# Kernel optimization log

Hardware: AMD Instinct MI355X
Metric: run time of the kernel (lower is better)

## Reference

```python
import jax, jax.numpy as jnp
import numpy as np

B, S, H = 2, 2048, 2048
E, I, SH = 8, 768, 5632
TOP_K = 2


def setup_inputs() -> dict:
    key = jax.random.key(0)
    ks = jax.random.split(key, 8)
    sc = lambda *shape: 1.0 / np.sqrt(shape[-2] if len(shape) > 1 else 1.0)
    return {
        "hidden_states": jax.random.normal(ks[0], (B, S, H), jnp.float32),
        "router_w": jax.random.normal(ks[1], (H, E), jnp.float32) * (1.0 / np.sqrt(H)),
        "expert_gate_up_w": jax.random.normal(ks[2], (E, H, 2 * I), jnp.float32) * (1.0 / np.sqrt(H)),
        "expert_down_w": jax.random.normal(ks[3], (E, I, H), jnp.float32) * (1.0 / np.sqrt(I)),
        "shared_gate_w": jax.random.normal(ks[4], (H, SH), jnp.float32) * (1.0 / np.sqrt(H)),
        "shared_up_w": jax.random.normal(ks[5], (H, SH), jnp.float32) * (1.0 / np.sqrt(H)),
        "shared_down_w": jax.random.normal(ks[6], (SH, H), jnp.float32) * (1.0 / np.sqrt(SH)),
        "shared_expert_gate_w": jax.random.normal(ks[7], (H, 1), jnp.float32) * (1.0 / np.sqrt(H)),
    }


def reference(hidden_states, router_w, expert_gate_up_w, expert_down_w,
              shared_gate_w, shared_up_w, shared_down_w, shared_expert_gate_w):
    b, s, h = hidden_states.shape
    x = hidden_states.reshape(-1, h)  # [T, H]

    # Shared expert (SwiGLU) gated by sigmoid scalar gate per token.
    gate = jax.nn.silu((x @ shared_gate_w).astype(jnp.float32)).astype(x.dtype)
    shared_out = (gate * (x @ shared_up_w)) @ shared_down_w  # [T, H]
    shared_out = jax.nn.sigmoid(x @ shared_expert_gate_w) * shared_out

    # Router: softmax -> top-k -> renormalize -> dense routing weights [E, T].
    router_logits = x @ router_w  # [T, E]
    router_probs = jax.nn.softmax(router_logits, axis=-1)
    top_p, top_i = jax.lax.top_k(router_probs, TOP_K)  # [T, k]
    top_p = top_p / jnp.sum(top_p, axis=-1, keepdims=True)
    one_hot = jax.nn.one_hot(top_i, E, dtype=top_p.dtype)  # [T, k, E]
    routing_full = jnp.sum(one_hot * top_p[..., None], axis=1)  # [T, E]
    routing_full = routing_full.T.astype(x.dtype)  # [E, T]

    # Dense per-expert SwiGLU over all tokens (as in source einsums).
    gate_up = jnp.einsum('th,ehm->etm', x, expert_gate_up_w)  # [E, T, 2I]
    g, u = jnp.split(gate_up, 2, axis=-1)
    g = jax.nn.silu(g.astype(jnp.float32)).astype(x.dtype)
    expert_out = jnp.einsum('eti,eih->eth', u * g, expert_down_w)  # [E, T, H]

    expert_contribution = jnp.sum(expert_out * routing_full[:, :, None], axis=0)  # [T, H]
    out = (expert_contribution + shared_out).reshape(b, s, h)
    return out, router_logits
```

## Files before the change

### kernel.cpp

```cpp
#include <hip/hip_runtime.h>
#include <hip/hip_bf16.h>
#include <stdint.h>

#define DEVFN static __device__ __forceinline__

typedef __attribute__((ext_vector_type(8))) short bf16x8;
typedef __attribute__((ext_vector_type(4))) float f32x4;
typedef unsigned short u16;
typedef unsigned int u32;
typedef unsigned long long u64;

DEVFN u16 f2bf(float f) {
    union { float f; u32 u; } v; v.f = f;
    u32 r = v.u + 0x7FFFu + ((v.u >> 16) & 1u);
    return (u16)(r >> 16);
}

DEVFN void g2l16(const void* g, void* l) {
    __builtin_amdgcn_global_load_lds(
        (const __attribute__((address_space(1))) u32*)g,
        (__attribute__((address_space(3))) u32*)l, 16, 0, 0);
}

template<int NSLOT>
DEVFN void stage(const u16* __restrict__ src, int ldk, u16* lds, int tid) {
#pragma unroll
    for (int i = 0; i < NSLOT / 256; ++i) {
        int slot = i * 256 + tid;
        int row = slot >> 2, chunk = slot & 3;
        int kg = chunk ^ ((row >> 1) & 3);
        g2l16(src + (long)row * ldk + kg * 8, lds + slot * 8);
    }
}

DEVFN bf16x8 ld_frag(const u16* lds, int row, int kg) {
    int chunk = kg ^ ((row >> 1) & 3);
    const u16* p = lds + row * 32 + chunk * 8;
    return *(const __attribute__((address_space(3))) bf16x8*)p;
}

__global__ __launch_bounds__(256) void gemm_down_k(
    const u16* __restrict__ A, const u16* __restrict__ B,
    float* __restrict__ C, const float* __restrict__ gvec,
    int K, int ldc)
{
    __shared__ u16 sm[2][8192];
    const int tid = threadIdx.x;
    const int lane = tid & 63, wv = tid >> 6;
    const int wm = wv >> 1, wn = wv & 1;
    const int m0 = blockIdx.y * 128, n0 = blockIdx.x * 128;
    const u16* Ab = A + (long)m0 * K;
    const u16* Bb = B + (long)n0 * K;

    f32x4 acc[4][4];
#pragma unroll
    for (int i = 0; i < 4; ++i)
#pragma unroll
        for (int j = 0; j < 4; ++j) acc[i][j] = f32x4{0.f, 0.f, 0.f, 0.f};

    stage<512>(Ab, K, &sm[0][0], tid);
    stage<512>(Bb, K, &sm[0][4096], tid);

    const int nk = K >> 5;
    for (int kt = 0; kt < nk; ++kt) {
        const int cur = kt & 1;
        __syncthreads();
        if (kt + 1 < nk) {
            stage<512>(Ab + (kt + 1) * 32, K, &sm[cur ^ 1][0], tid);
            stage<512>(Bb + (kt + 1) * 32, K, &sm[cur ^ 1][4096], tid);
        }
        const int l15 = lane & 15, kg = lane >> 4;
        bf16x8 av[4], bv[4];
#pragma unroll
        for (int f = 0; f < 4; ++f) {
            av[f] = ld_frag(&sm[cur][0],    wm * 64 + f * 16 + l15, kg);
            bv[f] = ld_frag(&sm[cur][4096], wn * 64 + f * 16 + l15, kg);
        }
#pragma unroll
        for (int fm = 0; fm < 4; ++fm)
#pragma unroll
            for (int fn = 0; fn < 4; ++fn)
                acc[fm][fn] = __builtin_amdgcn_mfma_f32_16x16x32_bf16(
                    av[fm], bv[fn], acc[fm][fn], 0, 0, 0);
    }

    const int l15 = lane & 15, lq = lane >> 4;
#pragma unroll
    for (int fm = 0; fm < 4; ++fm) {
#pragma unroll
        for (int j = 0; j < 4; ++j) {
            int row = m0 + wm * 64 + fm * 16 + lq * 4 + j;
            float gmul = gvec[row];
#pragma unroll
            for (int fn = 0; fn < 4; ++fn) {
                int col = n0 + wn * 64 + fn * 16 + l15;
                C[(long)row * ldc + col] = acc[fm][fn][j] * gmul;
            }
        }
    }
}

__global__ __launch_bounds__(256) void gemm_swiglu_k(
    const u16* __restrict__ A, const u16* __restrict__ Bg,
    const u16* __restrict__ Bu, u16* __restrict__ out, int K, int ldc)
{
    __shared__ u16 sm[2][8192];
    const int tid = threadIdx.x;
    const int lane = tid & 63, wv = tid >> 6;
    const int wm = wv >> 1, wn = wv & 1;
    const int m0 = blockIdx.y * 128, n0 = blockIdx.x * 64;
    const u16* Ab  = A  + (long)m0 * K;
    const u16* Bgb = Bg + (long)n0 * K;
    const u16* Bub = Bu + (long)n0 * K;

    f32x4 ag[4][2], au[4][2];
#pragma unroll
    for (int i = 0; i < 4; ++i)
#pragma unroll
        for (int j = 0; j < 2; ++j) {
            ag[i][j] = f32x4{0.f, 0.f, 0.f, 0.f};
            au[i][j] = f32x4{0.f, 0.f, 0.f, 0.f};
        }

    stage<512>(Ab,  K, &sm[0][0],    tid);
    stage<256>(Bgb, K, &sm[0][4096], tid);
    stage<256>(Bub, K, &sm[0][6144], tid);

    const int nk = K >> 5;
    for (int kt = 0; kt < nk; ++kt) {
        const int cur = kt & 1;
        __syncthreads();
        if (kt + 1 < nk) {
            stage<512>(Ab  + (kt + 1) * 32, K, &sm[cur ^ 1][0],    tid);
            stage<256>(Bgb + (kt + 1) * 32, K, &sm[cur ^ 1][4096], tid);
            stage<256>(Bub + (kt + 1) * 32, K, &sm[cur ^ 1][6144], tid);
        }
        const int l15 = lane & 15, kg = lane >> 4;
        bf16x8 av[4], gv[2], uv[2];
#pragma unroll
        for (int f = 0; f < 4; ++f)
            av[f] = ld_frag(&sm[cur][0], wm * 64 + f * 16 + l15, kg);
#pragma unroll
        for (int f = 0; f < 2; ++f) {
            gv[f] = ld_frag(&sm[cur][4096], wn * 32 + f * 16 + l15, kg);
            uv[f] = ld_frag(&sm[cur][6144], wn * 32 + f * 16 + l15, kg);
        }
#pragma unroll
        for (int fm = 0; fm < 4; ++fm)
#pragma unroll
            for (int fn = 0; fn < 2; ++fn) {
                ag[fm][fn] = __builtin_amdgcn_mfma_f32_16x16x32_bf16(
                    av[fm], gv[fn], ag[fm][fn], 0, 0, 0);
                au[fm][fn] = __builtin_amdgcn_mfma_f32_16x16x32_bf16(
                    av[fm], uv[fn], au[fm][fn], 0, 0, 0);
            }
    }

    const int l15 = lane & 15, lq = lane >> 4;
#pragma unroll
    for (int fm = 0; fm < 4; ++fm) {
#pragma unroll
        for (int j = 0; j < 4; ++j) {
            int row = m0 + wm * 64 + fm * 16 + lq * 4 + j;
#pragma unroll
            for (int fn = 0; fn < 2; ++fn) {
                int col = n0 + wn * 32 + fn * 16 + l15;
                float g = ag[fm][fn][j], u = au[fm][fn][j];
                float s = g * (1.f / (1.f + __expf(-g))) * u;
                out[(long)row * ldc + col] = f2bf(s);
            }
        }
    }
}

__global__ __launch_bounds__(256) void gemm_swiglu_moe_k(
    const u16* __restrict__ xb, const u16* __restrict__ Beg,
    const u16* __restrict__ Beu, const int* __restrict__ tok,
    const int* __restrict__ cntp, u16* __restrict__ eact,
    int K, int I_, int cap)
{
    const int e = blockIdx.z;
    const int m0 = blockIdx.y * 128;
    if (m0 >= cntp[e]) return;
    const int n0 = blockIdx.x * 64;

    __shared__ u16 sm[2][8192];
    const int tid = threadIdx.x;
    const int lane = tid & 63, wv = tid >> 6;
    const int wm = wv >> 1, wn = wv & 1;

    const int rA0 = tid >> 2, rA1 = 64 + (tid >> 2);
    const int* tseg = tok + (long)e * cap + m0;
    const long t0 = tseg[rA0], t1 = tseg[rA1];
    const int kg0 = (tid & 3) ^ ((rA0 >> 1) & 3);
    const int kg1 = (tid & 3) ^ ((rA1 >> 1) & 3);
    const u16* pa0 = xb + t0 * K + kg0 * 8;
    const u16* pa1 = xb + t1 * K + kg1 * 8;

    const u16* Bgb = Beg + ((long)e * I_ + n0) * K;
    const u16* Bub = Beu + ((long)e * I_ + n0) * K;

    f32x4 ag[4][2], au[4][2];
#pragma unroll
    for (int i = 0; i < 4; ++i)
#pragma unroll
        for (int j = 0; j < 2; ++j) {
            ag[i][j] = f32x4{0.f, 0.f, 0.f, 0.f};
            au[i][j] = f32x4{0.f, 0.f, 0.f, 0.f};
        }

    g2l16(pa0, &sm[0][(long)tid * 8]);
    g2l16(pa1, &sm[0][(long)(256 + tid) * 8]);
    stage<256>(Bgb, K, &sm[0][4096], tid);
    stage<256>(Bub, K, &sm[0][6144], tid);

    const int nk = K >> 5;
    for (int kt = 0; kt < nk; ++kt) {
        const int cur = kt & 1;
        __syncthreads();
        if (kt + 1 < nk) {
            g2l16(pa0 + (kt + 1) * 32, &sm[cur ^ 1][(long)tid * 8]);
            g2l16(pa1 + (kt + 1) * 32, &sm[cur ^ 1][(long)(256 + tid) * 8]);
            stage<256>(Bgb + (kt + 1) * 32, K, &sm[cur ^ 1][4096], tid);
            stage<256>(Bub + (kt + 1) * 32, K, &sm[cur ^ 1][6144], tid);
        }
        const int l15 = lane & 15, kg = lane >> 4;
        bf16x8 av[4], gv[2], uv[2];
#pragma unroll
        for (int f = 0; f < 4; ++f)
            av[f] = ld_frag(&sm[cur][0], wm * 64 + f * 16 + l15, kg);
#pragma unroll
        for (int f = 0; f < 2; ++f) {
            gv[f] = ld_frag(&sm[cur][4096], wn * 32 + f * 16 + l15, kg);
            uv[f] = ld_frag(&sm[cur][6144], wn * 32 + f * 16 + l15, kg);
        }
#pragma unroll
        for (int fm = 0; fm < 4; ++fm)
#pragma unroll
            for (int fn = 0; fn < 2; ++fn) {
                ag[fm][fn] = __builtin_amdgcn_mfma_f32_16x16x32_bf16(
                    av[fm], gv[fn], ag[fm][fn], 0, 0, 0);
                au[fm][fn] = __builtin_amdgcn_mfma_f32_16x16x32_bf16(
                    av[fm], uv[fn], au[fm][fn], 0, 0, 0);
            }
    }

    const int l15 = lane & 15, lq = lane >> 4;
#pragma unroll
    for (int fm = 0; fm < 4; ++fm) {
#pragma unroll
        for (int j = 0; j < 4; ++j) {
            long row = (long)e * cap + m0 + wm * 64 + fm * 16 + lq * 4 + j;
#pragma unroll
            for (int fn = 0; fn < 2; ++fn) {
                int col = n0 + wn * 32 + fn * 16 + l15;
                float g = ag[fm][fn][j], u = au[fm][fn][j];
                float s = g * (1.f / (1.f + __expf(-g))) * u;
                eact[row * I_ + col] = f2bf(s);
            }
        }
    }
}

__global__ __launch_bounds__(256) void gemm_down_moe_k(
    const u16* __restrict__ eact, const u16* __restrict__ Bed,
    float* __restrict__ out, const int* __restrict__ tok,
    const float* __restrict__ wrow, const int* __restrict__ cntp,
    int K, int ldc, int cap)
{
    const int e = blockIdx.z;
    const int m0 = blockIdx.y * 128;
    if (m0 >= cntp[e]) return;
    const int n0 = blockIdx.x * 128;

    __shared__ u16 sm[2][8192];
    const int tid = threadIdx.x;
    const int lane = tid & 63, wv = tid >> 6;
    const int wm = wv >> 1, wn = wv & 1;
    const u16* Ab = eact + ((long)e * cap + m0) * K;
    const u16* Bb = Bed + (long)e * ldc * K + (long)n0 * K;

    f32x4 acc[4][4];
#pragma unroll
    for (int i = 0; i < 4; ++i)
#pragma unroll
        for (int j = 0; j < 4; ++j) acc[i][j] = f32x4{0.f, 0.f, 0.f, 0.f};

    stage<512>(Ab, K, &sm[0][0], tid);
    stage<512>(Bb, K, &sm[0][4096], tid);

    const int nk = K >> 5;
    for (int kt = 0; kt < nk; ++kt) {
        const int cur = kt & 1;
        __syncthreads();
        if (kt + 1 < nk) {
            stage<512>(Ab + (kt + 1) * 32, K, &sm[cur ^ 1][0], tid);
            stage<512>(Bb + (kt + 1) * 32, K, &sm[cur ^ 1][4096], tid);
        }
        const int l15 = lane & 15, kg = lane >> 4;
        bf16x8 av[4], bv[4];
#pragma unroll
        for (int f = 0; f < 4; ++f) {
            av[f] = ld_frag(&sm[cur][0],    wm * 64 + f * 16 + l15, kg);
            bv[f] = ld_frag(&sm[cur][4096], wn * 64 + f * 16 + l15, kg);
        }
#pragma unroll
        for (int fm = 0; fm < 4; ++fm)
#pragma unroll
            for (int fn = 0; fn < 4; ++fn)
                acc[fm][fn] = __builtin_amdgcn_mfma_f32_16x16x32_bf16(
                    av[fm], bv[fn], acc[fm][fn], 0, 0, 0);
    }

    const int l15 = lane & 15, lq = lane >> 4;
#pragma unroll
    for (int fm = 0; fm < 4; ++fm) {
#pragma unroll
        for (int j = 0; j < 4; ++j) {
            long crow = (long)e * cap + m0 + wm * 64 + fm * 16 + lq * 4 + j;
            float w = wrow[crow];
            if (w != 0.f) {
                long t = tok[crow];
#pragma unroll
                for (int fn = 0; fn < 4; ++fn) {
                    int col = n0 + wn * 64 + fn * 16 + l15;
                    atomicAdd(out + t * ldc + col, acc[fm][fn][j] * w);
                }
            }
        }
    }
}

__global__ __launch_bounds__(256) void router_k(
    const float* __restrict__ x, const float* __restrict__ rw,
    const float* __restrict__ sgw, float* __restrict__ logits,
    int2* __restrict__ te, float2* __restrict__ tw,
    float* __restrict__ sig, int T, int H)
{
    const int tid = threadIdx.x, lane = tid & 63, wv = tid >> 6;
    const int t = blockIdx.x * 4 + wv;
    const float* xr = x + (long)t * H;
    float acc[8] = {0, 0, 0, 0, 0, 0, 0, 0};
    float as = 0.f;
    for (int h = lane; h < H; h += 64) {
        float xv = xr[h];
        const float* r = rw + h * 8;
#pragma unroll
        for (int e = 0; e < 8; ++e) acc[e] += xv * r[e];
        as += xv * sgw[h];
    }
#pragma unroll
    for (int off = 32; off; off >>= 1) {
#pragma unroll
        for (int e = 0; e < 8; ++e) acc[e] += __shfl_xor(acc[e], off);
        as += __shfl_xor(as, off);
    }
    if (lane == 0) {
        float mx = acc[0];
#pragma unroll
        for (int e = 1; e < 8; ++e) mx = fmaxf(mx, acc[e]);
        float p[8], sum = 0.f;
#pragma unroll
        for (int e = 0; e < 8; ++e) { p[e] = expf(acc[e] - mx); sum += p[e]; }
        int i1 = 0;
#pragma unroll
        for (int e = 1; e < 8; ++e) if (p[e] > p[i1]) i1 = e;
        int i2 = (i1 == 0) ? 1 : 0;
#pragma unroll
        for (int e = 0; e < 8; ++e) if (e != i1 && p[e] > p[i2]) i2 = e;
        float den = p[i1] + p[i2];
        te[t] = make_int2(i1, i2);
        tw[t] = make_float2(p[i1] / den, p[i2] / den);
#pragma unroll
        for (int e = 0; e < 8; ++e) logits[(long)t * 8 + e] = acc[e];
        sig[t] = 1.f / (1.f + expf(-as));
    }
}

__global__ __launch_bounds__(256) void compact_k(
    const int2* __restrict__ te, const float2* __restrict__ tw,
    int* __restrict__ tok, float* __restrict__ wrow,
    int* __restrict__ cntp, int T, int cap)
{
    const int e = blockIdx.x;
    const int tid = threadIdx.x, lane = tid & 63, wv = tid >> 6;
    __shared__ int wtot[4];
    int cnt = 0;
    for (int c0 = 0; c0 < T; c0 += 256) {
        int t = c0 + tid;
        int2 ids = te[t];
        float2 ws = tw[t];
        float w = (ids.x == e) ? ws.x : ((ids.y == e) ? ws.y : -1.f);
        bool sel = (w >= 0.f);
        u64 b = __ballot(sel);
        int rln = __popcll(b & ((1ull << lane) - 1ull));
        if (lane == 0) wtot[wv] = __popcll(b);
        __syncthreads();
        int rank = rln, tot = 0;
#pragma unroll
        for (int k = 0; k < 4; ++k) { if (k < wv) rank += wtot[k]; tot += wtot[k]; }
        if (sel) {
            int pos = cnt + rank;
            if (pos < cap) {
                tok[(long)e * cap + pos] = t;
                wrow[(long)e * cap + pos] = w;
            }
        }
        cnt += tot;
        __syncthreads();
    }
    if (cnt > cap) cnt = cap;
    int cp = (cnt + 127) & ~127;
    for (int p = cnt + tid; p < cp; p += 256) {
        tok[(long)e * cap + p] = 0;
        wrow[(long)e * cap + p] = 0.f;
    }
    if (tid == 0) cntp[e] = cp;
}

__global__ __launch_bounds__(256) void transpose_k(
    const float* __restrict__ src0, long src_zstr, int src_ld,
    u16* __restrict__ dst0, long dst_zstr, int dst_ld)
{
    __shared__ float tile[32][33];
    const float* src = src0 + (long)blockIdx.z * src_zstr;
    u16* dst = dst0 + (long)blockIdx.z * dst_zstr;
    int r0 = blockIdx.y * 32, c0 = blockIdx.x * 32;
    int tx = threadIdx.x, ty = threadIdx.y;
#pragma unroll
    for (int k = 0; k < 4; ++k)
        tile[ty + 8 * k][tx] = src[(long)(r0 + ty + 8 * k) * src_ld + c0 + tx];
    __syncthreads();
#pragma unroll
    for (int k = 0; k < 4; ++k)
        dst[(long)(c0 + ty + 8 * k) * dst_ld + r0 + tx] = f2bf(tile[tx][ty + 8 * k]);
}

__global__ __launch_bounds__(256) void cvt_x_k(const float* __restrict__ x,
                                               u16* __restrict__ xb)
{
    long i = ((long)blockIdx.x * 256 + threadIdx.x) * 4;
    float4 v = *(const float4*)(x + i);
    union { u16 s[4]; uint2 v2; } o;
    o.s[0] = f2bf(v.x); o.s[1] = f2bf(v.y); o.s[2] = f2bf(v.z); o.s[3] = f2bf(v.w);
    *(uint2*)(xb + i) = o.v2;
}

extern "C" void kernel_launch(void* const* d_in, const int* in_sizes, int n_in,
                              void* d_out, int out_size, void* d_ws, size_t ws_size,
                              hipStream_t stream) {
    (void)in_sizes; (void)n_in; (void)out_size; (void)ws_size;
    const int Hd = 2048, E = 8, I = 768, SH = 5632, T = 4096, CAP = 2048;

    const float* x    = (const float*)d_in[0];
    const float* rw   = (const float*)d_in[1];
    const float* egu  = (const float*)d_in[2];
    const float* edw  = (const float*)d_in[3];
    const float* sgw  = (const float*)d_in[4];
    const float* suw  = (const float*)d_in[5];
    const float* sdw  = (const float*)d_in[6];
    const float* segw = (const float*)d_in[7];
    float* out = (float*)d_out;
    float* logits = out + (size_t)T * Hd;

    char* wsp = (char*)d_ws;
    size_t off = 0;
    auto alloc = [&](size_t bytes) {
        void* p = wsp + off; off += (bytes + 255) & ~(size_t)255; return p;
    };
    u16* xb   = (u16*)alloc((size_t)T * Hd * 2);
    u16* Bgs  = (u16*)alloc((size_t)SH * Hd * 2);
    u16* Bus  = (u16*)alloc((size_t)SH * Hd * 2);
    u16* Bds  = (u16*)alloc((size_t)Hd * SH * 2);
    u16* Beg  = (u16*)alloc((size_t)E * I * Hd * 2);
    u16* Beu  = (u16*)alloc((size_t)E * I * Hd * 2);
    u16* Bed  = (u16*)alloc((size_t)E * Hd * I * 2);
    u16* hs   = (u16*)alloc((size_t)T * SH * 2);
    u16* eact = (u16*)alloc((size_t)E * CAP * I * 2);
    int2*   te   = (int2*)alloc((size_t)T * 8);
    float2* tw   = (float2*)alloc((size_t)T * 8);
    int*    tok  = (int*)alloc((size_t)E * CAP * 4);
    float*  wrow = (float*)alloc((size_t)E * CAP * 4);
    int*    cntp = (int*)alloc(64);
    float*  sig  = (float*)alloc((size_t)T * 4);

    dim3 tb(32, 8);
    cvt_x_k<<<(T * Hd) / 1024, 256, 0, stream>>>(x, xb);
    router_k<<<T / 4, 256, 0, stream>>>(x, rw, segw, logits, te, tw, sig, T, Hd);
    compact_k<<<E, 256, 0, stream>>>(te, tw, tok, wrow, cntp, T, CAP);

    transpose_k<<<dim3(SH / 32, Hd / 32), tb, 0, stream>>>(sgw, 0, SH, Bgs, 0, Hd);
    transpose_k<<<dim3(SH / 32, Hd / 32), tb, 0, stream>>>(suw, 0, SH, Bus, 0, Hd);
    transpose_k<<<dim3(Hd / 32, SH / 32), tb, 0, stream>>>(sdw, 0, Hd, Bds, 0, SH);
    transpose_k<<<dim3(I / 32, Hd / 32, E), tb, 0, stream>>>(
        egu, (long)Hd * 2 * I, 2 * I, Beg, (long)I * Hd, Hd);
    transpose_k<<<dim3(I / 32, Hd / 32, E), tb, 0, stream>>>(
        egu + I, (long)Hd * 2 * I, 2 * I, Beu, (long)I * Hd, Hd);
    transpose_k<<<dim3(Hd / 32, I / 32, E), tb, 0, stream>>>(
        edw, (long)I * Hd, Hd, Bed, (long)Hd * I, I);

    gemm_swiglu_k<<<dim3(SH / 64, T / 128), 256, 0, stream>>>(
        xb, Bgs, Bus, hs, Hd, SH);
    gemm_down_k<<<dim3(Hd / 128, T / 128), 256, 0, stream>>>(
        hs, Bds, out, sig, SH, Hd);
    gemm_swiglu_moe_k<<<dim3(I / 64, CAP / 128, E), 256, 0, stream>>>(
        xb, Beg, Beu, tok, cntp, eact, Hd, I, CAP);
    gemm_down_moe_k<<<dim3(Hd / 128, CAP / 128, E), 256, 0, stream>>>(
        eact, Bed, out, tok, wrow, cntp, I, Hd, CAP);
}
```

Before: 656.2 us.

## Replace shared-expert SwiGLU GEMM with 256x128 8-wave pipelined kernel

Replaces the 128x64 double-buffered shared-expert gate/up GEMM with an 8-wave, 256x128 tile kernel using K=64 steps. It uses 128KB of dynamic LDS, an XOR swizzle, and staggered half-tile async loads fenced by explicit vmcnt waits and barriers. It also adds s_setprio around the MFMA blocks and a block-index remap that groups neighbouring tiles. The goal is more data reuse per LDS byte and better overlap of global loads with MFMA. In exchange it relies on hand-tuned waitcnt ordering and drops to low occupancy.

Result: faster. 612.3 us (-6.7%).

```diff
diff --git a/kernel.cpp b/kernel.cpp
--- a/kernel.cpp
+++ b/kernel.cpp
@@ -20,6 +20,153 @@
     __builtin_amdgcn_global_load_lds(
         (const __attribute__((address_space(1))) u32*)g,
         (__attribute__((address_space(3))) u32*)l, 16, 0, 0);
+}
+
+DEVFN void hbar() {
+    __asm__ __volatile__("" ::: "memory");
+    __builtin_amdgcn_s_barrier();
+    __asm__ __volatile__("" ::: "memory");
+}
+DEVFN void vm4() { asm volatile("s_waitcnt vmcnt(4)" ::: "memory"); }
+DEVFN void vm0() { asm volatile("s_waitcnt vmcnt(0)" ::: "memory"); }
+
+__global__ __launch_bounds__(512, 2) void gemm8_swiglu_k(
+    const u16* __restrict__ A, const u16* __restrict__ Bg,
+    const u16* __restrict__ Bu, u16* __restrict__ out,
+    int K, int nx, int ldc)
+{
+    extern __shared__ char smraw[];
+    char* smA = smraw;
+    char* smB = smraw + 65536;
+
+    const int tid = threadIdx.x;
+    const int lane = tid & 63, wv = tid >> 6;
+    const int wm = wv >> 2, wn = wv & 3;
+    const int l15 = lane & 15, kg = lane >> 4;
+
+    const int nwg = gridDim.x;
+    const int id = (blockIdx.x & 7) * (nwg >> 3) + (blockIdx.x >> 3);
+    const int m0 = (id / nx) * 256, n0 = (id % nx) * 128;
+
+    const u16* Ap  = A  + (long)m0 * K;
+    const u16* Bgp = Bg + (long)n0 * K;
+    const u16* Bup = Bu + (long)n0 * K;
+
+    f32x4 accg[8][2], accu[8][2];
+#pragma unroll
+    for (int i = 0; i < 8; ++i)
+#pragma unroll
+        for (int j = 0; j < 2; ++j) {
+            accg[i][j] = f32x4{0.f, 0.f, 0.f, 0.f};
+            accu[i][j] = f32x4{0.f, 0.f, 0.f, 0.f};
+        }
+
+    auto stA = [&](int kt, int hh, int buf) {
+        const u16* src = Ap + ((long)hh * 128) * K + kt * 64;
+        char* dst = smA + buf * 32768 + hh * 16384;
+#pragma unroll
+        for (int i = 0; i < 2; ++i) {
+            int slot = i * 512 + tid;
+            int row = slot >> 3, ch = slot & 7;
+            g2l16(src + (long)row * K + ((ch ^ (row & 7)) << 3), dst + slot * 16);
+        }
+    };
+    auto stB = [&](int kt, int hh, int buf) {
+        const u16* src = (hh ? Bup : Bgp) + kt * 64;
+        char* dst = smB + buf * 32768 + hh * 16384;
+#pragma unroll
+        for (int i = 0; i < 2; ++i) {
+            int slot = i * 512 + tid;
+            int row = slot >> 3, ch = slot & 7;
+            g2l16(src + (long)row * K + ((ch ^ (row & 7)) << 3), dst + slot * 16);
+        }
+    };
+    auto frag = [&](const char* base, int r, int c) -> bf16x8 {
+        return *(const __attribute__((address_space(3))) bf16x8*)
+            (base + r * 128 + ((c ^ (r & 7)) << 4));
+    };
+
+    stA(0, 0, 0); stA(0, 1, 0);
+    stB(0, 0, 0); stB(0, 1, 0);
+    stB(1, 0, 1); stB(1, 1, 1);
+    vm4();
+    hbar();
+
+    const int nk = K >> 6;
+    for (int kt = 0; kt < nk; kt += 2) {
+        const bool more = (kt + 2) < nk;
+#pragma unroll
+        for (int h = 0; h < 2; ++h) {
+            const char* ab = smA + h * 32768;
+            const char* bb = smB + h * 32768;
+            bf16x8 bgv[2][2], buv[2][2];
+#pragma unroll
+            for (int p = 0; p < 4; ++p) {
+                if (p == 0) {
+#pragma unroll
+                    for (int fn = 0; fn < 2; ++fn)
+#pragma unroll
+                        for (int s = 0; s < 2; ++s) {
+                            int rB = wn * 32 + fn * 16 + l15;
+                            bgv[fn][s] = frag(bb, rB, s * 4 + kg);
+                            buv[fn][s] = frag(bb + 16384, rB, s * 4 + kg);
+                        }
+                }
+                bf16x8 av[2][2];
+#pragma unroll
+                for (int am = 0; am < 2; ++am)
+#pragma unroll
+                    for (int s = 0; s < 2; ++s)
+                        av[am][s] = frag(ab, wm * 128 + (p * 2 + am) * 16 + l15,
+                                         s * 4 + kg);
+                if (h == 0) {
+                    if (p == 0)      { stA(kt + 1, 0, 1); stA(kt + 1, 1, 1); }
+                    else if (p == 1) { if (more) stB(kt + 2, 0, 0); }
+                    else if (p == 2) { if (more) stB(kt + 2, 1, 0); }
+                    else             { if (more) vm4(); else vm0(); }
+                } else {
+                    if (more) {
+                        if (p == 0)      stA(kt + 2, 0, 0);
+                        else if (p == 1) stA(kt + 2, 1, 0);
+                        else if (p == 2) stB(kt + 3, 0, 1);
+                        else             { stB(kt + 3, 1, 1); vm4(); }
+                    }
+                }
+                hbar();
+                __builtin_amdgcn_sched_barrier(0);
+                __builtin_amdgcn_s_setprio(1);
+#pragma unroll
+                for (int am = 0; am < 2; ++am)
+#pragma unroll
+                    for (int s = 0; s < 2; ++s)
+#pragma unroll
+                        for (int fn = 0; fn < 2; ++fn) {
+                            accg[p * 2 + am][fn] = __builtin_amdgcn_mfma_f32_16x16x32_bf16(
+                                av[am][s], bgv[fn][s], accg[p * 2 + am][fn], 0, 0, 0);
+                            accu[p * 2 + am][fn] = __builtin_amdgcn_mfma_f32_16x16x32_bf16(
+                                av[am][s], buv[fn][s], accu[p * 2 + am][fn], 0, 0, 0);
+                        }
+                __builtin_amdgcn_s_setprio(0);
+                __builtin_amdgcn_sched_barrier(0);
+                hbar();
+            }
+        }
+    }
+
+    const int lq = lane >> 4;
+#pragma unroll
+    for (int fm = 0; fm < 8; ++fm)
+#pragma unroll
+        for (int j = 0; j < 4; ++j) {
+            int row = m0 + wm * 128 + fm * 16 + lq * 4 + j;
+#pragma unroll
+            for (int fn = 0; fn < 2; ++fn) {
+                int col = n0 + wn * 32 + fn * 16 + l15;
+                float g = accg[fm][fn][j], u = accu[fm][fn][j];
+                float s = g * (1.f / (1.f + __expf(-g))) * u;
+                out[(long)row * ldc + col] = f2bf(s);
+            }
+        }
 }
 
 template<int NSLOT>
@@ -95,79 +242,6 @@
             for (int fn = 0; fn < 4; ++fn) {
                 int col = n0 + wn * 64 + fn * 16 + l15;
                 C[(long)row * ldc + col] = acc[fm][fn][j] * gmul;
-            }
-        }
-    }
-}
-
-__global__ __launch_bounds__(256) void gemm_swiglu_k(
-    const u16* __restrict__ A, const u16* __restrict__ Bg,
-    const u16* __restrict__ Bu, u16* __restrict__ out, int K, int ldc)
-{
-    __shared__ u16 sm[2][8192];
-    const int tid = threadIdx.x;
-    const int lane = tid & 63, wv = tid >> 6;
-    const int wm = wv >> 1, wn = wv & 1;
-    const int m0 = blockIdx.y * 128, n0 = blockIdx.x * 64;
-    const u16* Ab  = A  + (long)m0 * K;
-    const u16* Bgb = Bg + (long)n0 * K;
-    const u16* Bub = Bu + (long)n0 * K;
-
-    f32x4 ag[4][2], au[4][2];
-#pragma unroll
-    for (int i = 0; i < 4; ++i)
-#pragma unroll
-        for (int j = 0; j < 2; ++j) {
-            ag[i][j] = f32x4{0.f, 0.f, 0.f, 0.f};
-            au[i][j] = f32x4{0.f, 0.f, 0.f, 0.f};
-        }
-
-    stage<512>(Ab,  K, &sm[0][0],    tid);
-    stage<256>(Bgb, K, &sm[0][4096], tid);
-    stage<256>(Bub, K, &sm[0][6144], tid);
-
-    const int nk = K >> 5;
-    for (int kt = 0; kt < nk; ++kt) {
-        const int cur = kt & 1;
-        __syncthreads();
-        if (kt + 1 < nk) {
-            stage<512>(Ab  + (kt + 1) * 32, K, &sm[cur ^ 1][0],    tid);
-            stage<256>(Bgb + (kt + 1) * 32, K, &sm[cur ^ 1][4096], tid);
-            stage<256>(Bub + (kt + 1) * 32, K, &sm[cur ^ 1][6144], tid);
-        }
-        const int l15 = lane & 15, kg = lane >> 4;
-        bf16x8 av[4], gv[2], uv[2];
-#pragma unroll
-        for (int f = 0; f < 4; ++f)
-            av[f] = ld_frag(&sm[cur][0], wm * 64 + f * 16 + l15, kg);
-#pragma unroll
-        for (int f = 0; f < 2; ++f) {
-            gv[f] = ld_frag(&sm[cur][4096], wn * 32 + f * 16 + l15, kg);
-            uv[f] = ld_frag(&sm[cur][6144], wn * 32 + f * 16 + l15, kg);
-        }
-#pragma unroll
-        for (int fm = 0; fm < 4; ++fm)
-#pragma unroll
-            for (int fn = 0; fn < 2; ++fn) {
-                ag[fm][fn] = __builtin_amdgcn_mfma_f32_16x16x32_bf16(
-                    av[fm], gv[fn], ag[fm][fn], 0, 0, 0);
-                au[fm][fn] = __builtin_amdgcn_mfma_f32_16x16x32_bf16(
-                    av[fm], uv[fn], au[fm][fn], 0, 0, 0);
-            }
-    }
-
-    const int l15 = lane & 15, lq = lane >> 4;
-#pragma unroll
-    for (int fm = 0; fm < 4; ++fm) {
-#pragma unroll
-        for (int j = 0; j < 4; ++j) {
-            int row = m0 + wm * 64 + fm * 16 + lq * 4 + j;
-#pragma unroll
-            for (int fn = 0; fn < 2; ++fn) {
-                int col = n0 + wn * 32 + fn * 16 + l15;
-                float g = ag[fm][fn][j], u = au[fm][fn][j];
-                float s = g * (1.f / (1.f + __expf(-g))) * u;
-                out[(long)row * ldc + col] = f2bf(s);
             }
         }
     }
@@ -484,6 +558,9 @@
     int*    cntp = (int*)alloc(64);
     float*  sig  = (float*)alloc((size_t)T * 4);
 
+    hipFuncSetAttribute((const void*)gemm8_swiglu_k,
+                        hipFuncAttributeMaxDynamicSharedMemorySize, 131072);
+
     dim3 tb(32, 8);
     cvt_x_k<<<(T * Hd) / 1024, 256, 0, stream>>>(x, xb);
     router_k<<<T / 4, 256, 0, stream>>>(x, rw, segw, logits, te, tw, sig, T, Hd);
@@ -499,8 +576,8 @@
     transpose_k<<<dim3(Hd / 32, I / 32, E), tb, 0, stream>>>(
         edw, (long)I * Hd, Hd, Bed, (long)Hd * I, I);
 
-    gemm_swiglu_k<<<dim3(SH / 64, T / 128), 256, 0, stream>>>(
-        xb, Bgs, Bus, hs, Hd, SH);
+    gemm8_swiglu_k<<<dim3((SH / 128) * (T / 256)), 512, 131072, stream>>>(
+        xb, Bgs, Bus, hs, Hd, SH / 128, SH);
     gemm_down_k<<<dim3(Hd / 128, T / 128), 256, 0, stream>>>(
         hs, Bds, out, sig, SH, Hd);
     gemm_swiglu_moe_k<<<dim3(I / 64, CAP / 128, E), 256, 0, stream>>>(
```
